# Kernel tuning notes

Hardware: AMD Instinct MI355X
Metric: run time of the kernel (lower is better)

## Reference

```python
import jax, jax.numpy as jnp
import numpy as np

EPSILON = 0.1
MAX_ITER = 100
THRESHOLD = 0.001
NORMALIZE = True
INPUT_SCALE = 0.02  # keeps exp(-cost/eps) from underflowing with randn inputs


def setup_inputs() -> dict:
    key = jax.random.key(0)
    k1, k2 = jax.random.split(key)
    compressed_tokens = jax.random.normal(k1, (16, 64, 768), dtype=jnp.float32) * INPUT_SCALE
    original_tokens = jax.random.normal(k2, (16, 1024, 768), dtype=jnp.float32) * INPUT_SCALE
    return {"compressed_tokens": compressed_tokens, "original_tokens": original_tokens}


def _cost_matrix(source, target):
    # pairwise squared Euclidean distances: (n, m)
    source_sq = jnp.sum(source ** 2, axis=1, keepdims=True)          # (n, 1)
    target_sq = jnp.sum(target ** 2, axis=1, keepdims=True)          # (m, 1)
    cross = source @ target.T                                         # (n, m)
    return source_sq + target_sq.T - 2.0 * cross


def _sinkhorn(K, a, b):
    n, m = K.shape
    u0 = jnp.ones((n,), K.dtype)
    v0 = jnp.ones((m,), K.dtype)

    def step(carry, _):
        u, v, done = carry
        u_new = a / (K @ v + 1e-10)
        v_new = b / (K.T @ u_new + 1e-10)
        err = jnp.max(jnp.abs(u_new - u))
        # torch breaks AFTER the update, so the converged u,v are post-update;
        # once done, freeze u,v (equivalent to breaking out of the loop)
        u_next = jnp.where(done, u, u_new)
        v_next = jnp.where(done, v, v_new)
        done_next = done | (err < THRESHOLD)
        return (u_next, v_next, done_next), None

    (u, v, _), _ = jax.lax.scan(step, (u0, v0, jnp.asarray(False)), None, length=MAX_ITER)
    return u, v


def reference(compressed_tokens, original_tokens):
    d = compressed_tokens.shape[-1]
    src = compressed_tokens.reshape(-1, d)   # (n, d)
    tgt = original_tokens.reshape(-1, d)     # (m, d)
    n, m = src.shape[0], tgt.shape[0]

    cost = _cost_matrix(src, tgt)            # (n, m)
    K = jnp.exp(-cost / EPSILON)
    a = jnp.full((n,), 1.0 / n, dtype=cost.dtype)
    b = jnp.full((m,), 1.0 / m, dtype=cost.dtype)

    u, v = _sinkhorn(K, a, b)

    # <P, C> with P = diag(u) K diag(v)
    ot_distance = jnp.sum((u[:, None] * K * v[None, :]) * cost)
    if NORMALIZE:
        ot_distance = ot_distance / (n + m)
    ot_loss = jnp.sqrt(ot_distance + 1e-8)
    return ot_loss
```

## Files before the change

kernel.cpp:

```cpp
#include <hip/hip_runtime.h>

#define NSRC 1024
#define MTGT 16384
#define DDIM 768
#define MAXIT 100
#define NBLK 256
#define NTHR 1024
#define NGRP 16
#define GRPSZ 16

typedef __attribute__((ext_vector_type(8))) short bf16x8;
typedef __attribute__((ext_vector_type(4))) float f32x4;
typedef __attribute__((ext_vector_type(4))) unsigned short u16x4;
typedef __attribute__((ext_vector_type(8))) unsigned short u16x8;

__device__ __forceinline__ unsigned short f2bf(float f) {
  unsigned u = __float_as_uint(f);
  u += 0x7FFFu + ((u >> 16) & 1u);
  return (unsigned short)(u >> 16);
}
__device__ __forceinline__ float bf2f(unsigned short h) {
  return __uint_as_float(((unsigned)h) << 16);
}
__device__ __forceinline__ void gstoref(float* p, float x) {
  __hip_atomic_store(p, x, __ATOMIC_RELAXED, __HIP_MEMORY_SCOPE_AGENT);
}
__device__ __forceinline__ float gloadf(const float* p) {
  return __hip_atomic_load(p, __ATOMIC_RELAXED, __HIP_MEMORY_SCOPE_AGENT);
}
__device__ __forceinline__ unsigned gloadu(const unsigned* p) {
  return __hip_atomic_load(p, __ATOMIC_RELAXED, __HIP_MEMORY_SCOPE_AGENT);
}

__global__ __launch_bounds__(256) void ot_prep_kernel(
    const float* __restrict__ src, unsigned short* __restrict__ Ab,
    float* __restrict__ ssq, unsigned* __restrict__ ctrl) {
  const int gid = blockIdx.x * 256 + threadIdx.x;
  #pragma unroll
  for (int k = 0; k < 3; ++k) {
    int idx = gid + k * 65536;
    float4 a = *(const float4*)(src + (size_t)idx * 4);
    u16x4 b; b[0] = f2bf(a.x); b[1] = f2bf(a.y); b[2] = f2bf(a.z); b[3] = f2bf(a.w);
    *(u16x4*)(Ab + (size_t)idx * 4) = b;
  }
  {
    int row = gid >> 6, l = gid & 63;
    float s = 0.f;
    #pragma unroll
    for (int k = 0; k < 3; ++k) {
      float4 a = *(const float4*)(src + (size_t)row * DDIM + (l + k * 64) * 4);
      s += a.x * a.x + a.y * a.y + a.z * a.z + a.w * a.w;
    }
    #pragma unroll
    for (int off = 32; off > 0; off >>= 1) s += __shfl_down(s, off, 64);
    if (l == 0) ssq[row] = s;
  }
  if (gid < 4096) ctrl[gid] = 0u;
}

__device__ __forceinline__ void grid_barrier(unsigned* garr, unsigned* root,
                                             unsigned* gen, unsigned& t) {
  __syncthreads();
  if (threadIdx.x == 0) {
    asm volatile("s_waitcnt vmcnt(0)" ::: "memory");
    unsigned g = (unsigned)(blockIdx.x >> 4);
    unsigned old = __hip_atomic_fetch_add(&garr[g * 64], 1u, __ATOMIC_RELAXED,
                                          __HIP_MEMORY_SCOPE_AGENT);
    if (old == t * GRPSZ + (GRPSZ - 1)) {
      unsigned r = __hip_atomic_fetch_add(root, 1u, __ATOMIC_RELAXED,
                                          __HIP_MEMORY_SCOPE_AGENT);
      if (r == t * NGRP + (NGRP - 1)) {
        __hip_atomic_store(gen, t + 1u, __ATOMIC_RELAXED, __HIP_MEMORY_SCOPE_AGENT);
      } else {
        while (gloadu(gen) < t + 1u) __builtin_amdgcn_s_sleep(1);
      }
    } else {
      while (gloadu(gen) < t + 1u) __builtin_amdgcn_s_sleep(1);
    }
    t += 1u;
  }
  __syncthreads();
}

__global__ __launch_bounds__(NTHR) void ot_fused_kernel(
    const float* __restrict__ tgt, const unsigned short* __restrict__ Ab,
    const float* __restrict__ ssq,
    float* Kvp, float* Kvf, float* otp, float* __restrict__ out,
    unsigned* garr, unsigned* root, unsigned* gen) {
  __shared__ __align__(16) unsigned short Ks[NSRC * 64];
  __shared__ __align__(16) unsigned short Bs[2][4096];
  __shared__ float ulds[NSRC];
  __shared__ float red[1104];
  __shared__ float vlds[64];
  __shared__ float tsql[64];
  __shared__ int sflag;

  const int tid = threadIdx.x, bid = blockIdx.x;
  const int w = tid >> 6, l = tid & 63;
  const int lr = l & 15, hi = l >> 4;
  const int m0 = w * 64;
  const size_t c0 = (size_t)bid * 64;
  const int rB = tid >> 4, kq = tid & 15;
  unsigned bt = 0;
  const float A_VAL = 1.0f / NSRC, B_VAL = 1.0f / MTGT;

  f32x4 acc[4][4];
  #pragma unroll
  for (int fi = 0; fi < 4; ++fi)
    #pragma unroll
    for (int fj = 0; fj < 4; ++fj) acc[fi][fj] = (f32x4){0.f, 0.f, 0.f, 0.f};

  float tsq_part = 0.f;
  {
    float4 bv = *(const float4*)(tgt + (c0 + rB) * DDIM + kq * 4);
    tsq_part += bv.x * bv.x + bv.y * bv.y + bv.z * bv.z + bv.w * bv.w;
    u16x4 bb; bb[0] = f2bf(bv.x); bb[1] = f2bf(bv.y); bb[2] = f2bf(bv.z); bb[3] = f2bf(bv.w);
    *(u16x4*)(&Bs[0][rB * 64 + (((kq >> 1) ^ (rB & 7)) << 3) + ((kq & 1) << 2)]) = bb;
  }
  __syncthreads();

  for (int kt = 0; kt < 12; ++kt) {
    float4 bv;
    if (kt < 11)
      bv = *(const float4*)(tgt + (c0 + rB) * DDIM + (kt + 1) * 64 + kq * 4);
    #pragma unroll
    for (int kc = 0; kc < 2; ++kc) {
      bf16x8 a[4];
      #pragma unroll
      for (int fi = 0; fi < 4; ++fi)
        a[fi] = *(const bf16x8*)(Ab + (size_t)(m0 + fi * 16 + lr) * DDIM +
                                 kt * 64 + kc * 32 + hi * 8);
      #pragma unroll
      for (int fj = 0; fj < 4; ++fj) {
        int rb = fj * 16 + lr;
        bf16x8 b = *(const bf16x8*)(&Bs[kt & 1][rb * 64 + ((((kc << 2) | hi) ^ (rb & 7)) << 3)]);
        #pragma unroll
        for (int fi = 0; fi < 4; ++fi)
          acc[fi][fj] = __builtin_amdgcn_mfma_f32_16x16x32_bf16(a[fi], b, acc[fi][fj], 0, 0, 0);
      }
    }
    if (kt < 11) {
      tsq_part += bv.x * bv.x + bv.y * bv.y + bv.z * bv.z + bv.w * bv.w;
      u16x4 bb; bb[0] = f2bf(bv.x); bb[1] = f2bf(bv.y); bb[2] = f2bf(bv.z); bb[3] = f2bf(bv.w);
      *(u16x4*)(&Bs[(kt + 1) & 1][rB * 64 + (((kq >> 1) ^ (rB & 7)) << 3) + ((kq & 1) << 2)]) = bb;
    }
    __syncthreads();
  }

  {
    float s = tsq_part;
    s += __shfl_xor(s, 1, 64); s += __shfl_xor(s, 2, 64);
    s += __shfl_xor(s, 4, 64); s += __shfl_xor(s, 8, 64);
    if (kq == 0) tsql[rB] = s;
  }
  __syncthreads();

  {
    const float SC = 14.426950408889634f;
    #pragma unroll
    for (int fi = 0; fi < 4; ++fi) {
      #pragma unroll
      for (int e = 0; e < 4; ++e) {
        int r = m0 + fi * 16 + hi * 4 + e;
        float sq = ssq[r];
        #pragma unroll
        for (int fj = 0; fj < 4; ++fj) {
          int c = fj * 16 + lr;
          float cost = sq + tsql[c] - 2.0f * acc[fi][fj][e];
          float k = exp2f(-SC * cost);
          Ks[r * 64 + (((c >> 3) ^ (r & 7)) << 3) + (c & 7)] = f2bf(k);
        }
      }
    }
  }
  if (tid < 64) vlds[tid] = 1.0f;
  __syncthreads();

  float uold = 1.0f;
  for (int it = 0; it < MAXIT; ++it) {
    {
      const int i = tid;
      float p = 0.f;
      #pragma unroll
      for (int lu = 0; lu < 8; ++lu) {
        int su = lu ^ (i & 7);
        u16x8 k8 = *(const u16x8*)(&Ks[i * 64 + su * 8]);
        float4 va = *(const float4*)(&vlds[lu * 8]);
        float4 vb = *(const float4*)(&vlds[lu * 8 + 4]);
        p += bf2f(k8[0]) * va.x + bf2f(k8[1]) * va.y +
             bf2f(k8[2]) * va.z + bf2f(k8[3]) * va.w +
             bf2f(k8[4]) * vb.x + bf2f(k8[5]) * vb.y +
             bf2f(k8[6]) * vb.z + bf2f(k8[7]) * vb.w;
      }
      gstoref(&Kvp[(size_t)bid * NSRC + tid], p);
    }
    grid_barrier(garr, root, gen, bt);
    {
      float s = gloadf(&Kvp[(size_t)(tid >> 2) * NSRC + (bid << 2) + (tid & 3)]);
      s += __shfl_xor(s, 4, 64);  s += __shfl_xor(s, 8, 64);
      s += __shfl_xor(s, 16, 64); s += __shfl_xor(s, 32, 64);
      if (l < 4) red[w * 4 + l] = s;
      __syncthreads();
      if (tid < 4) {
        float t = 0.f;
        #pragma unroll
        for (int g = 0; g < 16; ++g) t += red[g * 4 + tid];
        gstoref(&Kvf[(bid << 2) + tid], t);
      }
    }
    grid_barrier(garr, root, gen, bt);
    {
      float kv = gloadf(&Kvf[tid]);
      float un = A_VAL / (kv + 1e-10f);
      float d = fabsf(un - uold);
      #pragma unroll
      for (int off = 32; off > 0; off >>= 1) d = fmaxf(d, __shfl_xor(d, off, 64));
      if (l == 0) red[w] = d;
      ulds[tid] = un;
      uold = un;
    }
    __syncthreads();
    if (tid == 0) {
      float dm = red[0];
      #pragma unroll
      for (int k = 1; k < 16; ++k) dm = fmaxf(dm, red[k]);
      sflag = (dm < 0.001f) ? 1 : 0;
    }
    __syncthreads();
    const bool last = (sflag != 0) || (it == MAXIT - 1);

    {
      float* wred = (float*)Bs;
      const int c = l;
      float t = 0.f, ww = 0.f;
      #pragma unroll 8
      for (int r = 0; r < 64; ++r) {
        int i = w * 64 + r;
        float ui = ulds[i];
        float k = bf2f(Ks[i * 64 + (((c >> 3) ^ (i & 7)) << 3) + (c & 7)]);
        t += k * ui;
        if (last) ww += (k > 0.f) ? ui * k * (-0.1f * __logf(k)) : 0.f;
      }
      red[w * 68 + c] = t;
      if (last) wred[w * 68 + c] = ww;
      __syncthreads();
      if (tid < 64) {
        float tt = 0.f, wsum = 0.f;
        #pragma unroll
        for (int g = 0; g < 16; ++g) {
          tt += red[g * 68 + tid];
          if (last) wsum += wred[g * 68 + tid];
        }
        float vj = B_VAL / (tt + 1e-10f);
        vlds[tid] = vj;
        if (last) {
          float term = wsum * vj;
          #pragma unroll
          for (int off = 32; off > 0; off >>= 1) term += __shfl_down(term, off, 64);
          if (tid == 0) gstoref(&otp[bid], term);
        }
      }
    }
    __syncthreads();
    if (last) break;
  }

  grid_barrier(garr, root, gen, bt);
  if (bid == 0) {
    float s = (tid < NBLK) ? gloadf(&otp[tid]) : 0.f;
    if (tid < NBLK) {
      #pragma unroll
      for (int off = 32; off > 0; off >>= 1) s += __shfl_down(s, off, 64);
      if (l == 0) red[w] = s;
    }
    __syncthreads();
    if (tid == 0) {
      float tot = red[0] + red[1] + red[2] + red[3];
      out[0] = sqrtf(tot / (float)(NSRC + MTGT) + 1e-8f);
    }
  }
}

extern "C" void kernel_launch(void* const* d_in, const int* in_sizes, int n_in,
                              void* d_out, int out_size, void* d_ws, size_t ws_size,
                              hipStream_t stream) {
  const float* src = (const float*)d_in[0];
  const float* tgt = (const float*)d_in[1];
  float* out = (float*)d_out;
  char* ws = (char*)d_ws;

  unsigned short* Ab = (unsigned short*)(ws);
  float* ssq = (float*)(ws + 1572864);
  float* Kvp = (float*)(ws + 1576960);
  float* Kvf = (float*)(ws + 2625536);
  float* otp = (float*)(ws + 2629632);
  unsigned* ctrl = (unsigned*)(ws + 2630656);
  unsigned* garr = ctrl;
  unsigned* root = ctrl + 1024;
  unsigned* gen  = ctrl + 1040;

  ot_prep_kernel<<<256, 256, 0, stream>>>(src, Ab, ssq, ctrl);
  ot_fused_kernel<<<NBLK, NTHR, 0, stream>>>(tgt, Ab, ssq, Kvp, Kvf, otp, out,
                                             garr, root, gen);
}
```

Before: 178.5 us.

## Split fused kernel into GEMM and Sinkhorn kernels with K stored in global memory

The single persistent kernel becomes two. A GEMM kernel stages each block's whole target tile in LDS, computes the cost/exp matrix K, writes it as bf16 to global memory, and computes the first K·v with v=1 in its epilogue. The Sinkhorn kernel then streams K from global memory (about 32 MB, which may stay in cache) every iteration instead of keeping it in LDS. The loop is also reordered so that one grid barrier pass is skipped on the final iteration. The intent is to shorten the GEMM phase and free LDS, at the cost of repeated global or cache reads of K on each iteration and one extra kernel launch.

Result: slower. 253.4 us (+41.9%).

```diff
diff --git a/kernel.cpp b/kernel.cpp
--- a/kernel.cpp
+++ b/kernel.cpp
@@ -56,6 +56,99 @@
     if (l == 0) ssq[row] = s;
   }
   if (gid < 4096) ctrl[gid] = 0u;
+}
+
+__global__ __launch_bounds__(NTHR) void ot_gemm_kernel(
+    const float* __restrict__ tgt, const unsigned short* __restrict__ Ab,
+    const float* __restrict__ ssq,
+    unsigned short* __restrict__ Kb, float* __restrict__ Kvp) {
+  __shared__ __align__(16) unsigned short Bs[64 * 768];
+  __shared__ float tsql[64];
+  const int tid = threadIdx.x, bid = blockIdx.x;
+  const int w = tid >> 6, l = tid & 63;
+  const int lr = l & 15, hi = l >> 4;
+  const int m0 = w * 64;
+
+  #pragma unroll
+  for (int q = 0; q < 6; ++q) {
+    int idx2 = tid + q * 1024;
+    int rb = idx2 / 96, ch = idx2 % 96;
+    int kts = ch >> 3, m = ch & 7;
+    const float* gp = tgt + (size_t)(bid * 64 + rb) * DDIM + ch * 8;
+    float4 f0 = *(const float4*)gp;
+    float4 f1 = *(const float4*)(gp + 4);
+    u16x8 bb;
+    bb[0] = f2bf(f0.x); bb[1] = f2bf(f0.y); bb[2] = f2bf(f0.z); bb[3] = f2bf(f0.w);
+    bb[4] = f2bf(f1.x); bb[5] = f2bf(f1.y); bb[6] = f2bf(f1.z); bb[7] = f2bf(f1.w);
+    *(u16x8*)(&Bs[rb * 768 + (kts * 8 + (m ^ (rb & 7))) * 8]) = bb;
+  }
+  __syncthreads();
+
+  {
+    int rw = w * 4 + hi;
+    float s = 0.f;
+    #pragma unroll
+    for (int j = 0; j < 6; ++j) {
+      int ch = lr + j * 16;
+      int kts = ch >> 3, m = ch & 7;
+      u16x8 k8 = *(const u16x8*)(&Bs[rw * 768 + (kts * 8 + (m ^ (rw & 7))) * 8]);
+      #pragma unroll
+      for (int e = 0; e < 8; ++e) { float x = bf2f(k8[e]); s += x * x; }
+    }
+    s += __shfl_xor(s, 1, 64); s += __shfl_xor(s, 2, 64);
+    s += __shfl_xor(s, 4, 64); s += __shfl_xor(s, 8, 64);
+    if (lr == 0) tsql[rw] = s;
+  }
+
+  f32x4 acc[4][4];
+  #pragma unroll
+  for (int fi = 0; fi < 4; ++fi)
+    #pragma unroll
+    for (int fj = 0; fj < 4; ++fj) acc[fi][fj] = (f32x4){0.f, 0.f, 0.f, 0.f};
+
+  for (int kt = 0; kt < 12; ++kt) {
+    #pragma unroll
+    for (int kc = 0; kc < 2; ++kc) {
+      bf16x8 a[4], b[4];
+      #pragma unroll
+      for (int fi = 0; fi < 4; ++fi)
+        a[fi] = *(const bf16x8*)(Ab + (size_t)(m0 + fi * 16 + lr) * DDIM +
+                                 kt * 64 + kc * 32 + hi * 8);
+      #pragma unroll
+      for (int fj = 0; fj < 4; ++fj) {
+        int rb = fj * 16 + lr;
+        b[fj] = *(const bf16x8*)(&Bs[rb * 768 + (kt * 8 + ((kc * 4 + hi) ^ (rb & 7))) * 8]);
+      }
+      #pragma unroll
+      for (int fi = 0; fi < 4; ++fi)
+        #pragma unroll
+        for (int fj = 0; fj < 4; ++fj)
+          acc[fi][fj] = __builtin_amdgcn_mfma_f32_16x16x32_bf16(a[fi], b[fj], acc[fi][fj], 0, 0, 0);
+    }
+  }
+  __syncthreads();
+
+  const float SC = 14.426950408889634f;
+  #pragma unroll
+  for (int fi = 0; fi < 4; ++fi) {
+    #pragma unroll
+    for (int e = 0; e < 4; ++e) {
+      int row = m0 + fi * 16 + hi * 4 + e;
+      float sq = ssq[row];
+      float p = 0.f;
+      #pragma unroll
+      for (int fj = 0; fj < 4; ++fj) {
+        int col = bid * 64 + fj * 16 + lr;
+        float cost = sq + tsql[fj * 16 + lr] - 2.0f * acc[fi][fj][e];
+        float k = exp2f(-SC * cost);
+        Kb[(size_t)row * MTGT + col] = f2bf(k);
+        p += k;
+      }
+      p += __shfl_xor(p, 1, 64); p += __shfl_xor(p, 2, 64);
+      p += __shfl_xor(p, 4, 64); p += __shfl_xor(p, 8, 64);
+      if (lr == 0) Kvp[(size_t)bid * NSRC + row] = p;
+    }
+  }
 }
 
 __device__ __forceinline__ void grid_barrier(unsigned* garr, unsigned* root,
@@ -82,117 +175,125 @@
   __syncthreads();
 }
 
-__global__ __launch_bounds__(NTHR) void ot_fused_kernel(
-    const float* __restrict__ tgt, const unsigned short* __restrict__ Ab,
-    const float* __restrict__ ssq,
-    float* Kvp, float* Kvf, float* otp, float* __restrict__ out,
+__global__ __launch_bounds__(NTHR) void ot_sinkhorn_kernel(
+    const unsigned short* __restrict__ Kb, float* Kvp, float* Kvf,
+    float* otp, float* __restrict__ out,
     unsigned* garr, unsigned* root, unsigned* gen) {
-  __shared__ __align__(16) unsigned short Ks[NSRC * 64];
-  __shared__ __align__(16) unsigned short Bs[2][4096];
   __shared__ float ulds[NSRC];
-  __shared__ float red[1104];
   __shared__ float vlds[64];
-  __shared__ float tsql[64];
+  __shared__ float red[1088];
+  __shared__ float wred[1088];
   __shared__ int sflag;
-
   const int tid = threadIdx.x, bid = blockIdx.x;
   const int w = tid >> 6, l = tid & 63;
-  const int lr = l & 15, hi = l >> 4;
-  const int m0 = w * 64;
-  const size_t c0 = (size_t)bid * 64;
-  const int rB = tid >> 4, kq = tid & 15;
+  const int r8 = l >> 3, c8 = l & 7;
   unsigned bt = 0;
   const float A_VAL = 1.0f / NSRC, B_VAL = 1.0f / MTGT;
 
-  f32x4 acc[4][4];
-  #pragma unroll
-  for (int fi = 0; fi < 4; ++fi)
-    #pragma unroll
-    for (int fj = 0; fj < 4; ++fj) acc[fi][fj] = (f32x4){0.f, 0.f, 0.f, 0.f};
-
-  float tsq_part = 0.f;
   {
-    float4 bv = *(const float4*)(tgt + (c0 + rB) * DDIM + kq * 4);
-    tsq_part += bv.x * bv.x + bv.y * bv.y + bv.z * bv.z + bv.w * bv.w;
-    u16x4 bb; bb[0] = f2bf(bv.x); bb[1] = f2bf(bv.y); bb[2] = f2bf(bv.z); bb[3] = f2bf(bv.w);
-    *(u16x4*)(&Bs[0][rB * 64 + (((kq >> 1) ^ (rB & 7)) << 3) + ((kq & 1) << 2)]) = bb;
-  }
-  __syncthreads();
-
-  for (int kt = 0; kt < 12; ++kt) {
-    float4 bv;
-    if (kt < 11)
-      bv = *(const float4*)(tgt + (c0 + rB) * DDIM + (kt + 1) * 64 + kq * 4);
-    #pragma unroll
-    for (int kc = 0; kc < 2; ++kc) {
-      bf16x8 a[4];
-      #pragma unroll
-      for (int fi = 0; fi < 4; ++fi)
-        a[fi] = *(const bf16x8*)(Ab + (size_t)(m0 + fi * 16 + lr) * DDIM +
-                                 kt * 64 + kc * 32 + hi * 8);
-      #pragma unroll
-      for (int fj = 0; fj < 4; ++fj) {
-        int rb = fj * 16 + lr;
-        bf16x8 b = *(const bf16x8*)(&Bs[kt & 1][rb * 64 + ((((kc << 2) | hi) ^ (rb & 7)) << 3)]);
-        #pragma unroll
-        for (int fi = 0; fi < 4; ++fi)
-          acc[fi][fj] = __builtin_amdgcn_mfma_f32_16x16x32_bf16(a[fi], b, acc[fi][fj], 0, 0, 0);
-      }
-    }
-    if (kt < 11) {
-      tsq_part += bv.x * bv.x + bv.y * bv.y + bv.z * bv.z + bv.w * bv.w;
-      u16x4 bb; bb[0] = f2bf(bv.x); bb[1] = f2bf(bv.y); bb[2] = f2bf(bv.z); bb[3] = f2bf(bv.w);
-      *(u16x4*)(&Bs[(kt + 1) & 1][rB * 64 + (((kq >> 1) ^ (rB & 7)) << 3) + ((kq & 1) << 2)]) = bb;
-    }
-    __syncthreads();
-  }
-
-  {
-    float s = tsq_part;
-    s += __shfl_xor(s, 1, 64); s += __shfl_xor(s, 2, 64);
-    s += __shfl_xor(s, 4, 64); s += __shfl_xor(s, 8, 64);
-    if (kq == 0) tsql[rB] = s;
-  }
-  __syncthreads();
-
-  {
-    const float SC = 14.426950408889634f;
-    #pragma unroll
-    for (int fi = 0; fi < 4; ++fi) {
-      #pragma unroll
-      for (int e = 0; e < 4; ++e) {
-        int r = m0 + fi * 16 + hi * 4 + e;
-        float sq = ssq[r];
-        #pragma unroll
-        for (int fj = 0; fj < 4; ++fj) {
-          int c = fj * 16 + lr;
-          float cost = sq + tsql[c] - 2.0f * acc[fi][fj][e];
-          float k = exp2f(-SC * cost);
-          Ks[r * 64 + (((c >> 3) ^ (r & 7)) << 3) + (c & 7)] = f2bf(k);
-        }
-      }
-    }
-  }
-  if (tid < 64) vlds[tid] = 1.0f;
-  __syncthreads();
+    float s = gloadf(&Kvp[(size_t)(tid >> 2) * NSRC + (bid << 2) + (tid & 3)]);
+    s += __shfl_xor(s, 4, 64);  s += __shfl_xor(s, 8, 64);
+    s += __shfl_xor(s, 16, 64); s += __shfl_xor(s, 32, 64);
+    if (l < 4) red[w * 4 + l] = s;
+    __syncthreads();
+    if (tid < 4) {
+      float t = 0.f;
+      #pragma unroll
+      for (int g = 0; g < 16; ++g) t += red[g * 4 + tid];
+      gstoref(&Kvf[(bid << 2) + tid], t);
+    }
+  }
+  grid_barrier(garr, root, gen, bt);
 
   float uold = 1.0f;
   for (int it = 0; it < MAXIT; ++it) {
     {
-      const int i = tid;
-      float p = 0.f;
-      #pragma unroll
-      for (int lu = 0; lu < 8; ++lu) {
-        int su = lu ^ (i & 7);
-        u16x8 k8 = *(const u16x8*)(&Ks[i * 64 + su * 8]);
-        float4 va = *(const float4*)(&vlds[lu * 8]);
-        float4 vb = *(const float4*)(&vlds[lu * 8 + 4]);
-        p += bf2f(k8[0]) * va.x + bf2f(k8[1]) * va.y +
-             bf2f(k8[2]) * va.z + bf2f(k8[3]) * va.w +
-             bf2f(k8[4]) * vb.x + bf2f(k8[5]) * vb.y +
-             bf2f(k8[6]) * vb.z + bf2f(k8[7]) * vb.w;
-      }
-      gstoref(&Kvp[(size_t)bid * NSRC + tid], p);
+      float kv = gloadf(&Kvf[tid]);
+      float un = A_VAL / (kv + 1e-10f);
+      float d = fabsf(un - uold);
+      #pragma unroll
+      for (int off = 32; off > 0; off >>= 1) d = fmaxf(d, __shfl_xor(d, off, 64));
+      if (l == 0) red[w] = d;
+      ulds[tid] = un;
+      uold = un;
+    }
+    __syncthreads();
+    if (tid == 0) {
+      float dm = red[0];
+      #pragma unroll
+      for (int k = 1; k < 16; ++k) dm = fmaxf(dm, red[k]);
+      sflag = (dm < 0.001f) ? 1 : 0;
+    }
+    __syncthreads();
+    const bool last = (sflag != 0) || (it == MAXIT - 1);
+
+    {
+      float acc8[8], w8[8];
+      #pragma unroll
+      for (int e = 0; e < 8; ++e) { acc8[e] = 0.f; w8[e] = 0.f; }
+      #pragma unroll
+      for (int t = 0; t < 8; ++t) {
+        int i = w * 64 + t * 8 + r8;
+        float ui = ulds[i];
+        u16x8 k8 = *(const u16x8*)(Kb + (size_t)i * MTGT + bid * 64 + c8 * 8);
+        #pragma unroll
+        for (int e = 0; e < 8; ++e) {
+          float k = bf2f(k8[e]);
+          acc8[e] += k * ui;
+          if (last) w8[e] += (k > 0.f) ? ui * k * (-0.1f * __logf(k)) : 0.f;
+        }
+      }
+      #pragma unroll
+      for (int e = 0; e < 8; ++e) {
+        acc8[e] += __shfl_xor(acc8[e], 8, 64);
+        acc8[e] += __shfl_xor(acc8[e], 16, 64);
+        acc8[e] += __shfl_xor(acc8[e], 32, 64);
+        if (last) {
+          w8[e] += __shfl_xor(w8[e], 8, 64);
+          w8[e] += __shfl_xor(w8[e], 16, 64);
+          w8[e] += __shfl_xor(w8[e], 32, 64);
+        }
+      }
+      if (r8 == 0) {
+        #pragma unroll
+        for (int e = 0; e < 8; ++e) {
+          red[w * 68 + c8 * 8 + e] = acc8[e];
+          wred[w * 68 + c8 * 8 + e] = w8[e];
+        }
+      }
+      __syncthreads();
+      if (tid < 64) {
+        float tt = 0.f, wsum = 0.f;
+        #pragma unroll
+        for (int g = 0; g < 16; ++g) {
+          tt += red[g * 68 + tid];
+          if (last) wsum += wred[g * 68 + tid];
+        }
+        float vj = B_VAL / (tt + 1e-10f);
+        vlds[tid] = vj;
+        if (last) {
+          float term = wsum * vj;
+          #pragma unroll
+          for (int off = 32; off > 0; off >>= 1) term += __shfl_down(term, off, 64);
+          if (tid == 0) gstoref(&otp[bid], term);
+        }
+      }
+    }
+    __syncthreads();
+    if (last) break;
+
+    {
+      #pragma unroll
+      for (int t = 0; t < 8; ++t) {
+        int i = w * 64 + t * 8 + r8;
+        u16x8 k8 = *(const u16x8*)(Kb + (size_t)i * MTGT + bid * 64 + c8 * 8);
+        float p = bf2f(k8[0]) * vlds[c8 * 8 + 0] + bf2f(k8[1]) * vlds[c8 * 8 + 1] +
+                  bf2f(k8[2]) * vlds[c8 * 8 + 2] + bf2f(k8[3]) * vlds[c8 * 8 + 3] +
+                  bf2f(k8[4]) * vlds[c8 * 8 + 4] + bf2f(k8[5]) * vlds[c8 * 8 + 5] +
+                  bf2f(k8[6]) * vlds[c8 * 8 + 6] + bf2f(k8[7]) * vlds[c8 * 8 + 7];
+        p += __shfl_xor(p, 1, 64); p += __shfl_xor(p, 2, 64); p += __shfl_xor(p, 4, 64);
+        if (c8 == 0) gstoref(&Kvp[(size_t)bid * NSRC + i], p);
+      }
     }
     grid_barrier(garr, root, gen, bt);
     {
@@ -209,60 +310,6 @@
       }
     }
     grid_barrier(garr, root, gen, bt);
-    {
-      float kv = gloadf(&Kvf[tid]);
-      float un = A_VAL / (kv + 1e-10f);
-      float d = fabsf(un - uold);
-      #pragma unroll
-      for (int off = 32; off > 0; off >>= 1) d = fmaxf(d, __shfl_xor(d, off, 64));
-      if (l == 0) red[w] = d;
-      ulds[tid] = un;
-      uold = un;
-    }
-    __syncthreads();
-    if (tid == 0) {
-      float dm = red[0];
-      #pragma unroll
-      for (int k = 1; k < 16; ++k) dm = fmaxf(dm, red[k]);
-      sflag = (dm < 0.001f) ? 1 : 0;
-    }
-    __syncthreads();
-    const bool last = (sflag != 0) || (it == MAXIT - 1);
-
-    {
-      float* wred = (float*)Bs;
-      const int c = l;
-      float t = 0.f, ww = 0.f;
-      #pragma unroll 8
-      for (int r = 0; r < 64; ++r) {
-        int i = w * 64 + r;
-        float ui = ulds[i];
-        float k = bf2f(Ks[i * 64 + (((c >> 3) ^ (i & 7)) << 3) + (c & 7)]);
-        t += k * ui;
-        if (last) ww += (k > 0.f) ? ui * k * (-0.1f * __logf(k)) : 0.f;
-      }
-      red[w * 68 + c] = t;
-      if (last) wred[w * 68 + c] = ww;
-      __syncthreads();
-      if (tid < 64) {
-        float tt = 0.f, wsum = 0.f;
-        #pragma unroll
-        for (int g = 0; g < 16; ++g) {
-          tt += red[g * 68 + tid];
-          if (last) wsum += wred[g * 68 + tid];
-        }
-        float vj = B_VAL / (tt + 1e-10f);
-        vlds[tid] = vj;
-        if (last) {
-          float term = wsum * vj;
-          #pragma unroll
-          for (int off = 32; off > 0; off >>= 1) term += __shfl_down(term, off, 64);
-          if (tid == 0) gstoref(&otp[bid], term);
-        }
-      }
-    }
-    __syncthreads();
-    if (last) break;
   }
 
   grid_barrier(garr, root, gen, bt);
@@ -298,8 +345,10 @@
   unsigned* garr = ctrl;
   unsigned* root = ctrl + 1024;
   unsigned* gen  = ctrl + 1040;
+  unsigned short* Kb = (unsigned short*)(ws + 4194304);
 
   ot_prep_kernel<<<256, 256, 0, stream>>>(src, Ab, ssq, ctrl);
-  ot_fused_kernel<<<NBLK, NTHR, 0, stream>>>(tgt, Ab, ssq, Kvp, Kvf, otp, out,
-                                             garr, root, gen);
-}
+  ot_gemm_kernel<<<NBLK, NTHR, 0, stream>>>(tgt, Ab, ssq, Kb, Kvp);
+  ot_sinkhorn_kernel<<<NBLK, NTHR, 0, stream>>>(Kb, Kvp, Kvf, otp, out,
+                                                garr, root, gen);
+}
```
